# Kernel optimization log

Measured on AMD Instinct MI355X. Metric: run time of the kernel, lower is better.

Reference implementation:

```python
import jax, jax.numpy as jnp
import numpy as np

B, S, H, I, E, TOP_K, NS = 2, 2048, 2048, 1408, 8, 2, 2
SI = I * NS  # shared expert intermediate (intermediate_size * num_shared_expert)
INIT = 0.02


def setup_inputs() -> dict:
    key = jax.random.key(0)
    ks = jax.random.split(key, 9)
    f32 = jnp.float32
    return {
        "hidden_states": jax.random.normal(ks[0], (B, S, H), f32),
        # router classifier: Linear(H, E, bias=False), torch weight [E, H]
        "router_w": (jax.random.normal(ks[1], (E, H), f32) * INIT),
        # grouped experts (SwiGLU, no bias): [E, H, I], [E, H, I], [E, I, H]
        "gate_w": (jax.random.normal(ks[2], (E, H, I), f32) * INIT),
        "up_w": (jax.random.normal(ks[3], (E, H, I), f32) * INIT),
        "down_w": (jax.random.normal(ks[4], (E, I, H), f32) * INIT),
        # shared expert _MLP (bias=True), stored in matmul orientation
        "s_gate_w": (jax.random.normal(ks[5], (H, SI), f32) * INIT),
        "s_gate_b": jnp.zeros((SI,), f32),
        "s_up_w": (jax.random.normal(ks[6], (H, SI), f32) * INIT),
        "s_up_b": jnp.zeros((SI,), f32),
        "s_down_w": (jax.random.normal(ks[7], (SI, H), f32) * INIT),
        "s_down_b": jnp.zeros((H,), f32),
    }


def reference(hidden_states, router_w, gate_w, up_w, down_w,
              s_gate_w, s_gate_b, s_up_w, s_up_b, s_down_w, s_down_b):
    b, s, h = hidden_states.shape
    x = hidden_states.reshape(-1, h)          # [T, H]
    T = x.shape[0]
    num_experts = router_w.shape[0]

    # ---- router: logits -> fp32 softmax -> top-k -> renormalize ----
    logits = x @ router_w.T                   # [T, E]
    probs = jax.nn.softmax(logits.astype(jnp.float32), axis=-1)
    topk_w, topk_idx = jax.lax.top_k(probs, TOP_K)            # [T, K]
    topk_w = topk_w / jnp.sum(topk_w, axis=-1, keepdims=True)
    # dense combine weights [T, E]; zero for unrouted experts
    combine = jnp.zeros((T, num_experts), probs.dtype)
    combine = combine.at[jnp.arange(T)[:, None], topk_idx].add(topk_w)

    # ---- grouped SwiGLU experts; scan over E keeps peak memory at [T, I] ----
    def expert_step(acc, ws):
        gw, uw, dw, ce = ws                  # [H,I], [H,I], [I,H], [T]
        out = (jax.nn.silu(x @ gw) * (x @ uw)) @ dw           # [T, H]
        return acc + ce[:, None].astype(out.dtype) * out, None

    moe_out, _ = jax.lax.scan(expert_step, jnp.zeros_like(x),
                              (gate_w, up_w, down_w, combine.T))

    # ---- shared expert SwiGLU MLP (bias=True), overlapped -> added ----
    shared = (jax.nn.silu(x @ s_gate_w + s_gate_b)
              * (x @ s_up_w + s_up_b)) @ s_down_w + s_down_b

    return (moe_out + shared).reshape(b, s, h)
```

## Files before the change

kernel.cpp:

```cpp
#include <hip/hip_runtime.h>
#include <hip/hip_bf16.h>
#include <stdint.h>

#define T_TOK 4096
#define HDIM  2048
#define IDIM  1408
#define NEXP  8
#define SIDIM 2816
#define GU_CAP 781
#define DN_CAP 568

typedef __bf16 bf16_t;
typedef __bf16 bf16x8 __attribute__((ext_vector_type(8)));
typedef __bf16 bf16x4 __attribute__((ext_vector_type(4)));
typedef float  f32x4  __attribute__((ext_vector_type(4)));

typedef uint32_t __attribute__((address_space(3))) lds_u32;
typedef uint32_t __attribute__((address_space(1))) glb_u32;

__device__ __forceinline__ void glds16(const bf16_t* g, const char* l) {
  __builtin_amdgcn_global_load_lds((const glb_u32*)g, (lds_u32*)l, 16, 0, 0);
}

__device__ __forceinline__ void bar() {
  asm volatile("" ::: "memory");
  __builtin_amdgcn_s_barrier();
  asm volatile("" ::: "memory");
}
#define VMW4 asm volatile("s_waitcnt vmcnt(4)" ::: "memory")
#define VMW0 asm volatile("s_waitcnt vmcnt(0)" ::: "memory")

__device__ __forceinline__ int xcd_swz(int orig, int nwg) {
  int q = nwg >> 3, r = nwg & 7;
  int x = orig & 7, i = orig >> 3;
  return (x < r ? x * (q + 1) : r * (q + 1) + (x - r) * q) + i;
}

__global__ void cvt_x_kernel(const float4* __restrict__ in, bf16x4* __restrict__ out, int n4) {
  int i = blockIdx.x * 256 + threadIdx.x;
  if (i >= n4) return;
  float4 v = in[i];
  bf16x4 o;
  o[0] = (bf16_t)v.x; o[1] = (bf16_t)v.y; o[2] = (bf16_t)v.z; o[3] = (bf16_t)v.w;
  out[i] = o;
}

__global__ void tcvt_kernel(const float* __restrict__ in, bf16_t* __restrict__ out, int R, int C) {
  in  += (size_t)blockIdx.z * R * C;
  out += (size_t)blockIdx.z * R * C;
  __shared__ bf16_t tb[64][72];
  const int r0 = blockIdx.y * 64, c0 = blockIdx.x * 64;
  const int tid = threadIdx.x;
  const int cf4 = tid & 15, rr = tid >> 4;
#pragma unroll
  for (int s = 0; s < 4; ++s) {
    int r = rr + 16 * s;
    float4 v = *(const float4*)(in + (size_t)(r0 + r) * C + c0 + cf4 * 4);
    tb[cf4 * 4 + 0][r] = (bf16_t)v.x;
    tb[cf4 * 4 + 1][r] = (bf16_t)v.y;
    tb[cf4 * 4 + 2][r] = (bf16_t)v.z;
    tb[cf4 * 4 + 3][r] = (bf16_t)v.w;
  }
  __syncthreads();
  const int c = tid >> 2, rb = (tid & 3) * 16;
  bf16x8 w0 = *(const bf16x8*)&tb[c][rb];
  bf16x8 w1 = *(const bf16x8*)&tb[c][rb + 8];
  bf16_t* op = out + (size_t)(c0 + c) * R + r0 + rb;
  *(bf16x8*)op = w0;
  *(bf16x8*)(op + 8) = w1;
}

__global__ void tcvt_gu_kernel(const float* __restrict__ in, bf16_t* __restrict__ out,
                               int R, int C, int which) {
  in  += (size_t)blockIdx.z * R * C;
  out += (size_t)blockIdx.z * (2 * C) * R;
  __shared__ bf16_t tb[64][72];
  const int r0 = blockIdx.y * 64, c0 = blockIdx.x * 64;
  const int tid = threadIdx.x;
  const int cf4 = tid & 15, rr = tid >> 4;
#pragma unroll
  for (int s = 0; s < 4; ++s) {
    int r = rr + 16 * s;
    float4 v = *(const float4*)(in + (size_t)(r0 + r) * C + c0 + cf4 * 4);
    tb[cf4 * 4 + 0][r] = (bf16_t)v.x;
    tb[cf4 * 4 + 1][r] = (bf16_t)v.y;
    tb[cf4 * 4 + 2][r] = (bf16_t)v.z;
    tb[cf4 * 4 + 3][r] = (bf16_t)v.w;
  }
  __syncthreads();
  const int c = tid >> 2, rb = (tid & 3) * 16;
  bf16x8 w0 = *(const bf16x8*)&tb[c][rb];
  bf16x8 w1 = *(const bf16x8*)&tb[c][rb + 8];
  int cg = c0 + c;
  int nprime = ((cg >> 4) << 5) + which * 16 + (cg & 15);
  bf16_t* op = out + (size_t)nprime * R + r0 + rb;
  *(bf16x8*)op = w0;
  *(bf16x8*)(op + 8) = w1;
}

__global__ void router_kernel(const float* __restrict__ x, const float* __restrict__ rw,
                              int* __restrict__ tk_i, float* __restrict__ tk_w,
                              int* __restrict__ counts) {
  int gtid = blockIdx.x * 256 + threadIdx.x;
  int t = gtid >> 6, lane = gtid & 63;
  const float4* xr = (const float4*)(x + (size_t)t * HDIM);
  float acc[NEXP];
#pragma unroll
  for (int e = 0; e < NEXP; e++) acc[e] = 0.f;
  for (int i = lane; i < HDIM / 4; i += 64) {
    float4 xv = xr[i];
#pragma unroll
    for (int e = 0; e < NEXP; e++) {
      float4 wv = ((const float4*)(rw + e * HDIM))[i];
      acc[e] += xv.x * wv.x + xv.y * wv.y + xv.z * wv.z + xv.w * wv.w;
    }
  }
#pragma unroll
  for (int e = 0; e < NEXP; e++)
#pragma unroll
    for (int off = 32; off; off >>= 1) acc[e] += __shfl_down(acc[e], off);
  if (lane == 0) {
    int i1 = 0; float m1 = acc[0];
#pragma unroll
    for (int e = 1; e < NEXP; e++) if (acc[e] > m1) { m1 = acc[e]; i1 = e; }
    int i2 = -1; float m2 = -1e30f;
#pragma unroll
    for (int e = 0; e < NEXP; e++) if (e != i1 && acc[e] > m2) { m2 = acc[e]; i2 = e; }
    float w1 = 1.f / (1.f + __expf(m2 - m1));
    tk_i[t * 2] = i1; tk_i[t * 2 + 1] = i2;
    tk_w[t * 2] = w1; tk_w[t * 2 + 1] = 1.f - w1;
    atomicAdd(&counts[i1], 1); atomicAdd(&counts[i2], 1);
  }
}

__global__ void build_kernel(int* __restrict__ meta) {
  __shared__ int snmt;
  if (threadIdx.x == 0) {
    int o = 0;
    for (int e = 0; e < NEXP; e++) { meta[16 + e] = o; o += meta[e]; }
    meta[24] = o;
    int nmt = 0;
    for (int e = 0; e < NEXP; e++) {
      int nt = (meta[e] + 255) >> 8;
      for (int i = 0; i < nt; i++) { meta[32 + nmt] = e; meta[80 + nmt] = i << 8; nmt++; }
    }
    meta[25] = nmt;
    meta[26] = nmt * 11 + 352;
    meta[27] = nmt * 8 + 256;
    snmt = nmt;
  }
  __syncthreads();
  const int nmt = snmt;
  int4* gt = (int4*)(meta + 128);
  const int ng = nmt * 11 + 352;
  for (int i = threadIdx.x; i < ng; i += 256) {
    int4 v; v.w = 0;
    if (i < nmt * 11) {
      int xt = i / nmt, yt = i - xt * nmt;
      v.x = 0 | (meta[32 + yt] << 1); v.y = meta[80 + yt]; v.z = xt * 256;
    } else {
      int k = i - nmt * 11; int xt = k >> 4, yt = k & 15;
      v.x = 1; v.y = yt * 256; v.z = xt * 256;
    }
    gt[i] = v;
  }
  int4* dt4 = (int4*)(meta + 3328);
  const int nd = nmt * 8 + 256;
  for (int i = threadIdx.x; i < nd; i += 256) {
    int4 v; v.w = 0;
    if (i < nmt * 8) {
      int xt = i / nmt, yt = i - xt * nmt;
      v.x = 0 | (meta[32 + yt] << 1); v.y = meta[80 + yt]; v.z = xt * 256;
    } else {
      int k = i - nmt * 8; int xt = k >> 5, rem = k & 31, ks = rem >> 4, yt = rem & 15;
      v.x = 1 | (ks << 4); v.y = yt * 256; v.z = xt * 256;
    }
    dt4[i] = v;
  }
}

__global__ void scatter_kernel(const int* __restrict__ tk_i, const float* __restrict__ tk_w,
                               int* __restrict__ meta, int* __restrict__ tok_idx,
                               int* __restrict__ tk_slot) {
  int t = blockIdx.x * 256 + threadIdx.x;
  if (t >= T_TOK) return;
#pragma unroll
  for (int k = 0; k < 2; k++) {
    int e = tk_i[t * 2 + k];
    int pos = meta[16 + e] + atomicAdd(&meta[8 + e], 1);
    tok_idx[pos] = t; tk_slot[t * 2 + k] = pos;
  }
}

template <int OP>
__global__ __launch_bounds__(512, 2)
void gemm8p(const bf16_t* __restrict__ A0, const bf16_t* __restrict__ A1,
            const bf16_t* __restrict__ B0, const bf16_t* __restrict__ B1,
            bf16_t* __restrict__ O0, bf16_t* __restrict__ O1, bf16_t* __restrict__ O2,
            const float* __restrict__ bg, const float* __restrict__ bu,
            const int* __restrict__ meta, const int* __restrict__ tok_idx) {
  const int ntiles = meta[OP == 0 ? 26 : 27];
  const int l = blockIdx.x;
  if (l >= ntiles) return;
  const int s = xcd_swz(l, ntiles);
  const int4 tv = ((const int4*)(meta + (OP == 0 ? 128 : 3328)))[s];
  const int kind = tv.x & 1, e = (tv.x >> 1) & 7, ks = (tv.x >> 4) & 1;
  const int row0 = tv.y, n0 = tv.z;

  int cnt, slot0 = 0, strideA, strideB, koffA = 0, koffB = 0;
  const bf16_t *Ab, *Bp;
  constexpr int NKT = (OP == 0) ? (HDIM / 64) : (IDIM / 64);
  if (OP == 0) {
    strideA = HDIM; strideB = HDIM; Ab = A0;
    if (kind == 0) {
      slot0 = meta[16 + e]; cnt = meta[17 + e] - slot0;
      Bp = B0 + (size_t)e * (2 * IDIM) * HDIM;
    } else { cnt = T_TOK; Bp = B1; }
  } else {
    if (kind == 0) {
      slot0 = meta[16 + e]; cnt = meta[17 + e] - slot0;
      Ab = A0; strideA = IDIM;
      Bp = B0 + (size_t)e * HDIM * IDIM; strideB = IDIM;
    } else {
      cnt = T_TOK; Ab = A1; strideA = SIDIM; koffA = ks * IDIM;
      Bp = B1; strideB = SIDIM; koffB = ks * IDIM;
    }
  }

  __shared__ __align__(16) char smem[131072];

  const int t = threadIdx.x;
  const int lane = t & 63, wid = t >> 6;
  const int wr = wid >> 2, wc = wid & 3;
  const int lr = lane & 15, lg = lane >> 4;

  const bf16_t* pA[4]; const bf16_t* pB[4]; int dG[4];
#pragma unroll
  for (int j = 0; j < 4; ++j) {
    int g = j * 512 + t;
    int r = g >> 3;
    int c16 = (g & 7) ^ (r & 7);
    dG[j] = g * 16;
    int rr = row0 + r;
    if (kind == 0 && rr >= cnt) rr = cnt - 1;
    int arow;
    if (OP == 0 && kind == 0) arow = tok_idx[slot0 + rr];
    else if (OP == 1 && kind == 0) arow = slot0 + rr;
    else arow = rr;
    pA[j] = Ab + (size_t)arow * strideA + koffA + c16 * 8;
    pB[j] = Bp + (size_t)(n0 + r) * strideB + koffB + c16 * 8;
  }

  const int cswz0 = ((lg) ^ (lr & 7)) * 16;
  const int cswz1 = ((4 + lg) ^ (lr & 7)) * 16;
  const int aRowB = (wr * 128 + lr) * 128;
  const int bRowB = (wc * 64 + lr) * 128 + 65536;

  f32x4 acc[8][4];
#pragma unroll
  for (int mi = 0; mi < 8; ++mi)
#pragma unroll
    for (int ni = 0; ni < 4; ++ni) acc[mi][ni] = (f32x4)(0.f);

  bf16x8 aL[4][2], aH[4][2], bL[2][2], bH[2][2];

#define ST_A(BUFO, KT, JH) { \
    glds16(pA[(JH)*2]   + (KT)*64, smem + (BUFO) + dG[(JH)*2]); \
    glds16(pA[(JH)*2+1] + (KT)*64, smem + (BUFO) + dG[(JH)*2+1]); }
#define ST_B(BUFO, KT, JH) { \
    glds16(pB[(JH)*2]   + (KT)*64, smem + 65536 + (BUFO) + dG[(JH)*2]); \
    glds16(pB[(JH)*2+1] + (KT)*64, smem + 65536 + (BUFO) + dG[(JH)*2+1]); }
#define RD_A(af, BUFO, MIH) { \
    _Pragma("unroll") for (int mi = 0; mi < 4; ++mi) { \
      af[mi][0] = *(const bf16x8*)(smem + (BUFO) + aRowB + (MIH)*8192 + mi*2048 + cswz0); \
      af[mi][1] = *(const bf16x8*)(smem + (BUFO) + aRowB + (MIH)*8192 + mi*2048 + cswz1); } }
#define RD_B(bf, BUFO, NIH) { \
    _Pragma("unroll") for (int ni = 0; ni < 2; ++ni) { \
      bf[ni][0] = *(const bf16x8*)(smem + (BUFO) + bRowB + (NIH)*4096 + ni*2048 + cswz0); \
      bf[ni][1] = *(const bf16x8*)(smem + (BUFO) + bRowB + (NIH)*4096 + ni*2048 + cswz1); } }
#define MMQ(af, bf, MO, NO) { \
    __builtin_amdgcn_s_setprio(1); \
    _Pragma("unroll") for (int ni = 0; ni < 2; ++ni) \
    _Pragma("unroll") for (int mi = 0; mi < 4; ++mi) { \
      acc[(MO)+mi][(NO)+ni] = __builtin_amdgcn_mfma_f32_16x16x32_bf16(af[mi][0], bf[ni][0], acc[(MO)+mi][(NO)+ni], 0, 0, 0); \
      acc[(MO)+mi][(NO)+ni] = __builtin_amdgcn_mfma_f32_16x16x32_bf16(af[mi][1], bf[ni][1], acc[(MO)+mi][(NO)+ni], 0, 0, 0); } \
    __builtin_amdgcn_s_setprio(0); }
#define KTILE(KT, BO, NBO, W) { \
    RD_A(aL, BO, 0); RD_B(bL, BO, 0); \
    if ((KT) + 1 < NKT) ST_B(NBO, (KT) + 1, 0); \
    bar(); MMQ(aL, bL, 0, 0); bar(); \
    RD_A(aH, BO, 1); \
    if ((KT) + 1 < NKT) ST_B(NBO, (KT) + 1, 1); \
    bar(); MMQ(aH, bL, 4, 0); bar(); \
    RD_B(bH, BO, 1); \
    if ((KT) + 2 < NKT) ST_A(BO, (KT) + 2, 0); \
    bar(); MMQ(aH, bH, 4, 2); bar(); \
    if ((KT) + 2 < NKT) ST_A(BO, (KT) + 2, 1); \
    bar(); MMQ(aL, bH, 0, 2); \
    W; bar(); }

  ST_A(0, 0, 0); ST_A(0, 0, 1);
  ST_B(0, 0, 0); ST_B(0, 0, 1);
  ST_A(32768, 1, 0); ST_A(32768, 1, 1);
  VMW4; bar();

  for (int kt = 0; kt < NKT - 2; kt += 2) {
    KTILE(kt, 0, 32768, VMW4);
    KTILE(kt + 1, 32768, 0, VMW4);
  }
  KTILE(NKT - 2, 0, 32768, VMW0);
  KTILE(NKT - 1, 32768, 0, VMW0);

  if (OP == 0) {
    bf16_t* Ho = kind ? O1 : O0;
    const int HN = kind ? SIDIM : IDIM;
    const int Lbase = n0 >> 1;
#pragma unroll
    for (int mi = 0; mi < 8; ++mi)
#pragma unroll
      for (int j = 0; j < 4; ++j) {
        int row = wr * 128 + mi * 16 + lg * 4 + j;
        int grow = row0 + row;
        if (kind == 0 && grow >= cnt) continue;
        size_t orow = (size_t)((kind ? 0 : slot0) + grow);
#pragma unroll
        for (int nih = 0; nih < 2; ++nih) {
          int Lr = wc * 32 + nih * 16 + lr;
          float g = acc[mi][2 * nih][j];
          float u = acc[mi][2 * nih + 1][j];
          if (kind) { g += bg[Lbase + Lr]; u += bu[Lbase + Lr]; }
          float h = (g / (1.f + __expf(-g))) * u;
          Ho[orow * HN + Lbase + Lr] = (bf16_t)h;
        }
      }
  } else {
    bf16_t* Po = kind ? (ks ? O2 : O1) : O0;
#pragma unroll
    for (int mi = 0; mi < 8; ++mi)
#pragma unroll
      for (int j = 0; j < 4; ++j) {
        int row = wr * 128 + mi * 16 + lg * 4 + j;
        int grow = row0 + row;
        if (kind == 0 && grow >= cnt) continue;
        size_t orow = (size_t)((kind ? 0 : slot0) + grow);
#pragma unroll
        for (int ni = 0; ni < 4; ++ni) {
          int col = n0 + wc * 64 + ni * 16 + lr;
          Po[orow * HDIM + col] = (bf16_t)acc[mi][ni][j];
        }
      }
  }
#undef ST_A
#undef ST_B
#undef RD_A
#undef RD_B
#undef MMQ
#undef KTILE
}

__global__ void combine_kernel(const bf16_t* __restrict__ sh0, const bf16_t* __restrict__ sh1,
                               const bf16_t* __restrict__ rt, const int* __restrict__ tk_slot,
                               const float* __restrict__ tk_w, const float* __restrict__ sdb,
                               float* __restrict__ out) {
  const int t = blockIdx.x;
  const int c = threadIdx.x * 8;
  const int s1 = tk_slot[2 * t], s2 = tk_slot[2 * t + 1];
  const float w1 = tk_w[2 * t], w2 = tk_w[2 * t + 1];
  bf16x8 a = *(const bf16x8*)(sh0 + (size_t)t * HDIM + c);
  bf16x8 b = *(const bf16x8*)(sh1 + (size_t)t * HDIM + c);
  bf16x8 r1 = *(const bf16x8*)(rt + (size_t)s1 * HDIM + c);
  bf16x8 r2 = *(const bf16x8*)(rt + (size_t)s2 * HDIM + c);
  float4 d0 = *(const float4*)(sdb + c);
  float4 d1 = *(const float4*)(sdb + c + 4);
  float o[8];
#pragma unroll
  for (int i = 0; i < 8; i++)
    o[i] = (float)a[i] + (float)b[i] + w1 * (float)r1[i] + w2 * (float)r2[i];
  o[0] += d0.x; o[1] += d0.y; o[2] += d0.z; o[3] += d0.w;
  o[4] += d1.x; o[5] += d1.y; o[6] += d1.z; o[7] += d1.w;
  float4* op = (float4*)(out + (size_t)t * HDIM + c);
  op[0] = make_float4(o[0], o[1], o[2], o[3]);
  op[1] = make_float4(o[4], o[5], o[6], o[7]);
}

extern "C" void kernel_launch(void* const* d_in, const int* in_sizes, int n_in,
                              void* d_out, int out_size, void* d_ws, size_t ws_size,
                              hipStream_t stream) {
  const float* x_f  = (const float*)d_in[0];
  const float* rw   = (const float*)d_in[1];
  const float* gate = (const float*)d_in[2];
  const float* up   = (const float*)d_in[3];
  const float* down = (const float*)d_in[4];
  const float* sgw  = (const float*)d_in[5];
  const float* sgb  = (const float*)d_in[6];
  const float* suw  = (const float*)d_in[7];
  const float* sub  = (const float*)d_in[8];
  const float* sdw  = (const float*)d_in[9];
  const float* sdb  = (const float*)d_in[10];
  float* out = (float*)d_out;

  char* ws = (char*)d_ws;
  size_t off = 0;
  auto alloc = [&](size_t bytes) {
    char* p = ws + off;
    off += (bytes + 255) & ~(size_t)255;
    return p;
  };
  bf16_t* xb    = (bf16_t*)alloc((size_t)T_TOK * HDIM * 2);
  char*   bgur  = alloc((size_t)NEXP * 2 * IDIM * HDIM * 2);
  bf16_t* BguR  = (bf16_t*)bgur;
  bf16_t* BguS  = (bf16_t*)alloc((size_t)2 * SIDIM * HDIM * 2);
  bf16_t* dT    = (bf16_t*)alloc((size_t)NEXP * HDIM * IDIM * 2);
  bf16_t* sdT   = (bf16_t*)alloc((size_t)HDIM * SIDIM * 2);
  bf16_t* hid_r = (bf16_t*)alloc((size_t)(T_TOK * 2) * IDIM * 2);
  bf16_t* hid_s = (bf16_t*)alloc((size_t)T_TOK * SIDIM * 2);
  int*    meta  = (int*)alloc(32768);
  int*    tok_idx = (int*)alloc(8192 * 4);
  int*    tk_slot = (int*)alloc(8192 * 4);
  int*    tk_i    = (int*)alloc((size_t)T_TOK * 2 * 4);
  float*  tk_w2   = (float*)alloc((size_t)T_TOK * 2 * 4);

  bf16_t* rt_p  = (bf16_t*)bgur;
  bf16_t* sh_p0 = (bf16_t*)(bgur + (size_t)8192 * HDIM * 2);
  bf16_t* sh_p1 = (bf16_t*)(bgur + (size_t)8192 * HDIM * 2 + (size_t)T_TOK * HDIM * 2);

  hipMemsetAsync(meta, 0, 64, stream);

  cvt_x_kernel<<<(T_TOK * HDIM / 4) / 256, 256, 0, stream>>>(
      (const float4*)x_f, (bf16x4*)xb, T_TOK * HDIM / 4);

  tcvt_gu_kernel<<<dim3(IDIM / 64, HDIM / 64, NEXP), 256, 0, stream>>>(gate, BguR, HDIM, IDIM, 0);
  tcvt_gu_kernel<<<dim3(IDIM / 64, HDIM / 64, NEXP), 256, 0, stream>>>(up,   BguR, HDIM, IDIM, 1);
  tcvt_gu_kernel<<<dim3(SIDIM / 64, HDIM / 64, 1), 256, 0, stream>>>(sgw, BguS, HDIM, SIDIM, 0);
  tcvt_gu_kernel<<<dim3(SIDIM / 64, HDIM / 64, 1), 256, 0, stream>>>(suw, BguS, HDIM, SIDIM, 1);
  tcvt_kernel<<<dim3(HDIM / 64, IDIM / 64, NEXP), 256, 0, stream>>>(down, dT, IDIM, HDIM);
  tcvt_kernel<<<dim3(HDIM / 64, SIDIM / 64, 1), 256, 0, stream>>>(sdw, sdT, SIDIM, HDIM);

  router_kernel<<<T_TOK / 4, 256, 0, stream>>>(x_f, rw, tk_i, tk_w2, meta);
  build_kernel<<<1, 256, 0, stream>>>(meta);
  scatter_kernel<<<T_TOK / 256, 256, 0, stream>>>(tk_i, tk_w2, meta, tok_idx, tk_slot);

  gemm8p<0><<<GU_CAP, 512, 0, stream>>>(
      xb, nullptr, BguR, BguS, hid_r, hid_s, nullptr, sgb, sub, meta, tok_idx);
  gemm8p<1><<<DN_CAP, 512, 0, stream>>>(
      hid_r, hid_s, dT, sdT, rt_p, sh_p0, sh_p1, nullptr, nullptr, meta, nullptr);
  combine_kernel<<<T_TOK, 256, 0, stream>>>(sh_p0, sh_p1, rt_p, tk_slot, tk_w2, sdb, out);
}
```

Before: 622.0 us.

## Fuse down-weight transposes into gate/up GEMM and x-cast into router

The x fp32→bf16 cast moves into the router kernel, which already reads x, so one pass over x and one launch go away. The two down-projection transpose kernels become extra tile kinds (220 tiles of 64 rows each) in the gate/up GEMM's persistent tile list, so they run alongside the GEMM tiles. The down GEMM now uses a fixed 512-block persistent grid with a grid-stride loop over tiles. This removes several launches and lets the weight transposes overlap GEMM work, at the cost of larger tile metadata, re-encoded tile flags, and transpose tiles that leave MFMA units idle on the CUs that run them.

```diff
diff --git a/kernel.cpp b/kernel.cpp
--- a/kernel.cpp
+++ b/kernel.cpp
@@ -7,8 +7,9 @@
 #define IDIM  1408
 #define NEXP  8
 #define SIDIM 2816
-#define GU_CAP 781
-#define DN_CAP 568
+#define NCVT  220
+#define GU_CAP (781 + NCVT)
+#define DN_GRID 512
 
 typedef __bf16 bf16_t;
 typedef __bf16 bf16x8 __attribute__((ext_vector_type(8)));
@@ -34,40 +35,6 @@
   int q = nwg >> 3, r = nwg & 7;
   int x = orig & 7, i = orig >> 3;
   return (x < r ? x * (q + 1) : r * (q + 1) + (x - r) * q) + i;
-}
-
-__global__ void cvt_x_kernel(const float4* __restrict__ in, bf16x4* __restrict__ out, int n4) {
-  int i = blockIdx.x * 256 + threadIdx.x;
-  if (i >= n4) return;
-  float4 v = in[i];
-  bf16x4 o;
-  o[0] = (bf16_t)v.x; o[1] = (bf16_t)v.y; o[2] = (bf16_t)v.z; o[3] = (bf16_t)v.w;
-  out[i] = o;
-}
-
-__global__ void tcvt_kernel(const float* __restrict__ in, bf16_t* __restrict__ out, int R, int C) {
-  in  += (size_t)blockIdx.z * R * C;
-  out += (size_t)blockIdx.z * R * C;
-  __shared__ bf16_t tb[64][72];
-  const int r0 = blockIdx.y * 64, c0 = blockIdx.x * 64;
-  const int tid = threadIdx.x;
-  const int cf4 = tid & 15, rr = tid >> 4;
-#pragma unroll
-  for (int s = 0; s < 4; ++s) {
-    int r = rr + 16 * s;
-    float4 v = *(const float4*)(in + (size_t)(r0 + r) * C + c0 + cf4 * 4);
-    tb[cf4 * 4 + 0][r] = (bf16_t)v.x;
-    tb[cf4 * 4 + 1][r] = (bf16_t)v.y;
-    tb[cf4 * 4 + 2][r] = (bf16_t)v.z;
-    tb[cf4 * 4 + 3][r] = (bf16_t)v.w;
-  }
-  __syncthreads();
-  const int c = tid >> 2, rb = (tid & 3) * 16;
-  bf16x8 w0 = *(const bf16x8*)&tb[c][rb];
-  bf16x8 w1 = *(const bf16x8*)&tb[c][rb + 8];
-  bf16_t* op = out + (size_t)(c0 + c) * R + r0 + rb;
-  *(bf16x8*)op = w0;
-  *(bf16x8*)(op + 8) = w1;
 }
 
 __global__ void tcvt_gu_kernel(const float* __restrict__ in, bf16_t* __restrict__ out,
@@ -99,16 +66,21 @@
 }
 
 __global__ void router_kernel(const float* __restrict__ x, const float* __restrict__ rw,
+                              bf16_t* __restrict__ xb,
                               int* __restrict__ tk_i, float* __restrict__ tk_w,
                               int* __restrict__ counts) {
   int gtid = blockIdx.x * 256 + threadIdx.x;
   int t = gtid >> 6, lane = gtid & 63;
   const float4* xr = (const float4*)(x + (size_t)t * HDIM);
+  bf16x4* xo = (bf16x4*)(xb + (size_t)t * HDIM);
   float acc[NEXP];
 #pragma unroll
   for (int e = 0; e < NEXP; e++) acc[e] = 0.f;
   for (int i = lane; i < HDIM / 4; i += 64) {
     float4 xv = xr[i];
+    bf16x4 o;
+    o[0] = (bf16_t)xv.x; o[1] = (bf16_t)xv.y; o[2] = (bf16_t)xv.z; o[3] = (bf16_t)xv.w;
+    xo[i] = o;
 #pragma unroll
     for (int e = 0; e < NEXP; e++) {
       float4 wv = ((const float4*)(rw + e * HDIM))[i];
@@ -145,35 +117,40 @@
       for (int i = 0; i < nt; i++) { meta[32 + nmt] = e; meta[80 + nmt] = i << 8; nmt++; }
     }
     meta[25] = nmt;
-    meta[26] = nmt * 11 + 352;
+    meta[26] = nmt * 11 + 352 + NCVT;
     meta[27] = nmt * 8 + 256;
     snmt = nmt;
   }
   __syncthreads();
   const int nmt = snmt;
   int4* gt = (int4*)(meta + 128);
-  const int ng = nmt * 11 + 352;
+  const int ngemm = nmt * 11 + 352;
+  const int ng = ngemm + NCVT;
   for (int i = threadIdx.x; i < ng; i += 256) {
     int4 v; v.w = 0;
     if (i < nmt * 11) {
       int xt = i / nmt, yt = i - xt * nmt;
-      v.x = 0 | (meta[32 + yt] << 1); v.y = meta[80 + yt]; v.z = xt * 256;
-    } else {
+      v.x = 0 | (meta[32 + yt] << 3); v.y = meta[80 + yt]; v.z = xt * 256;
+    } else if (i < ngemm) {
       int k = i - nmt * 11; int xt = k >> 4, yt = k & 15;
       v.x = 1; v.y = yt * 256; v.z = xt * 256;
+    } else {
+      int k = i - ngemm;
+      if (k < 176) { v.x = 2 | ((k / 22) << 3); v.y = (k % 22) * 64; v.z = 0; }
+      else         { v.x = 2 | (1 << 2);        v.y = (k - 176) * 64; v.z = 0; }
     }
     gt[i] = v;
   }
-  int4* dt4 = (int4*)(meta + 3328);
+  int4* dt4 = (int4*)(meta + 4352);
   const int nd = nmt * 8 + 256;
   for (int i = threadIdx.x; i < nd; i += 256) {
     int4 v; v.w = 0;
     if (i < nmt * 8) {
       int xt = i / nmt, yt = i - xt * nmt;
-      v.x = 0 | (meta[32 + yt] << 1); v.y = meta[80 + yt]; v.z = xt * 256;
+      v.x = 0 | (meta[32 + yt] << 3); v.y = meta[80 + yt]; v.z = xt * 256;
     } else {
       int k = i - nmt * 8; int xt = k >> 5, rem = k & 31, ks = rem >> 4, yt = rem & 15;
-      v.x = 1 | (ks << 4); v.y = yt * 256; v.z = xt * 256;
+      v.x = 1 | (ks << 2); v.y = yt * 256; v.z = xt * 256;
     }
     dt4[i] = v;
   }
@@ -198,71 +175,101 @@
             const bf16_t* __restrict__ B0, const bf16_t* __restrict__ B1,
             bf16_t* __restrict__ O0, bf16_t* __restrict__ O1, bf16_t* __restrict__ O2,
             const float* __restrict__ bg, const float* __restrict__ bu,
-            const int* __restrict__ meta, const int* __restrict__ tok_idx) {
+            const int* __restrict__ meta, const int* __restrict__ tok_idx,
+            const float* __restrict__ W0, const float* __restrict__ W1,
+            bf16_t* __restrict__ D0, bf16_t* __restrict__ D1) {
+  __shared__ __align__(16) char smem[131072];
   const int ntiles = meta[OP == 0 ? 26 : 27];
-  const int l = blockIdx.x;
-  if (l >= ntiles) return;
-  const int s = xcd_swz(l, ntiles);
-  const int4 tv = ((const int4*)(meta + (OP == 0 ? 128 : 3328)))[s];
-  const int kind = tv.x & 1, e = (tv.x >> 1) & 7, ks = (tv.x >> 4) & 1;
-  const int row0 = tv.y, n0 = tv.z;
-
-  int cnt, slot0 = 0, strideA, strideB, koffA = 0, koffB = 0;
-  const bf16_t *Ab, *Bp;
-  constexpr int NKT = (OP == 0) ? (HDIM / 64) : (IDIM / 64);
-  if (OP == 0) {
-    strideA = HDIM; strideB = HDIM; Ab = A0;
-    if (kind == 0) {
-      slot0 = meta[16 + e]; cnt = meta[17 + e] - slot0;
-      Bp = B0 + (size_t)e * (2 * IDIM) * HDIM;
-    } else { cnt = T_TOK; Bp = B1; }
-  } else {
-    if (kind == 0) {
-      slot0 = meta[16 + e]; cnt = meta[17 + e] - slot0;
-      Ab = A0; strideA = IDIM;
-      Bp = B0 + (size_t)e * HDIM * IDIM; strideB = IDIM;
-    } else {
-      cnt = T_TOK; Ab = A1; strideA = SIDIM; koffA = ks * IDIM;
-      Bp = B1; strideB = SIDIM; koffB = ks * IDIM;
-    }
-  }
-
-  __shared__ __align__(16) char smem[131072];
-
   const int t = threadIdx.x;
   const int lane = t & 63, wid = t >> 6;
   const int wr = wid >> 2, wc = wid & 3;
   const int lr = lane & 15, lg = lane >> 4;
-
-  const bf16_t* pA[4]; const bf16_t* pB[4]; int dG[4];
-#pragma unroll
-  for (int j = 0; j < 4; ++j) {
-    int g = j * 512 + t;
-    int r = g >> 3;
-    int c16 = (g & 7) ^ (r & 7);
-    dG[j] = g * 16;
-    int rr = row0 + r;
-    if (kind == 0 && rr >= cnt) rr = cnt - 1;
-    int arow;
-    if (OP == 0 && kind == 0) arow = tok_idx[slot0 + rr];
-    else if (OP == 1 && kind == 0) arow = slot0 + rr;
-    else arow = rr;
-    pA[j] = Ab + (size_t)arow * strideA + koffA + c16 * 8;
-    pB[j] = Bp + (size_t)(n0 + r) * strideB + koffB + c16 * 8;
-  }
-
   const int cswz0 = ((lg) ^ (lr & 7)) * 16;
   const int cswz1 = ((4 + lg) ^ (lr & 7)) * 16;
   const int aRowB = (wr * 128 + lr) * 128;
   const int bRowB = (wc * 64 + lr) * 128 + 65536;
-
-  f32x4 acc[8][4];
-#pragma unroll
-  for (int mi = 0; mi < 8; ++mi)
-#pragma unroll
-    for (int ni = 0; ni < 4; ++ni) acc[mi][ni] = (f32x4)(0.f);
-
-  bf16x8 aL[4][2], aH[4][2], bL[2][2], bH[2][2];
+  constexpr int NKT = (OP == 0) ? (HDIM / 64) : (IDIM / 64);
+
+  for (int l = blockIdx.x; l < ntiles; l += gridDim.x) {
+    const int s = xcd_swz(l, ntiles);
+    const int4 tv = ((const int4*)(meta + (OP == 0 ? 128 : 4352)))[s];
+    const int kind = tv.x & 3, e = (tv.x >> 3) & 7, ks = (tv.x >> 2) & 1;
+    const int row0 = tv.y, n0 = tv.z;
+
+    if (OP == 0 && kind == 2) {
+      const float* src; bf16_t* dst; int Rst;
+      if (ks == 0) { src = W0 + ((size_t)e * IDIM + row0) * HDIM;
+                     dst = D0 + (size_t)e * HDIM * IDIM + row0; Rst = IDIM; }
+      else         { src = W1 + (size_t)row0 * HDIM; dst = D1 + row0; Rst = SIDIM; }
+      const int h = t >> 8, tid2 = t & 255;
+      bf16_t (*tb)[72] = (bf16_t(*)[72])(smem + h * 9216);
+      const int cf4 = tid2 & 15, rr2 = tid2 >> 4;
+      const int cc = tid2 >> 2, rb = (tid2 & 3) * 16;
+      for (int it = 0; it < 16; ++it) {
+        const int c0 = it * 128 + h * 64;
+        __syncthreads();
+#pragma unroll
+        for (int sdx = 0; sdx < 4; ++sdx) {
+          int r = rr2 + 16 * sdx;
+          float4 v = *(const float4*)(src + (size_t)r * HDIM + c0 + cf4 * 4);
+          tb[cf4 * 4 + 0][r] = (bf16_t)v.x;
+          tb[cf4 * 4 + 1][r] = (bf16_t)v.y;
+          tb[cf4 * 4 + 2][r] = (bf16_t)v.z;
+          tb[cf4 * 4 + 3][r] = (bf16_t)v.w;
+        }
+        __syncthreads();
+        bf16x8 w0 = *(const bf16x8*)&tb[cc][rb];
+        bf16x8 w1 = *(const bf16x8*)&tb[cc][rb + 8];
+        bf16_t* op = dst + (size_t)(c0 + cc) * Rst + rb;
+        *(bf16x8*)op = w0;
+        *(bf16x8*)(op + 8) = w1;
+      }
+      continue;
+    }
+
+    int cnt, slot0 = 0, strideA, strideB, koffA = 0, koffB = 0;
+    const bf16_t *Ab, *Bp;
+    if (OP == 0) {
+      strideA = HDIM; strideB = HDIM; Ab = A0;
+      if (kind == 0) {
+        slot0 = meta[16 + e]; cnt = meta[17 + e] - slot0;
+        Bp = B0 + (size_t)e * (2 * IDIM) * HDIM;
+      } else { cnt = T_TOK; Bp = B1; }
+    } else {
+      if (kind == 0) {
+        slot0 = meta[16 + e]; cnt = meta[17 + e] - slot0;
+        Ab = A0; strideA = IDIM;
+        Bp = B0 + (size_t)e * HDIM * IDIM; strideB = IDIM;
+      } else {
+        cnt = T_TOK; Ab = A1; strideA = SIDIM; koffA = ks * IDIM;
+        Bp = B1; strideB = SIDIM; koffB = ks * IDIM;
+      }
+    }
+
+    const bf16_t* pA[4]; const bf16_t* pB[4]; int dG[4];
+#pragma unroll
+    for (int j = 0; j < 4; ++j) {
+      int g = j * 512 + t;
+      int r = g >> 3;
+      int c16 = (g & 7) ^ (r & 7);
+      dG[j] = g * 16;
+      int rr = row0 + r;
+      if (kind == 0 && rr >= cnt) rr = cnt - 1;
+      int arow;
+      if (OP == 0 && kind == 0) arow = tok_idx[slot0 + rr];
+      else if (OP == 1 && kind == 0) arow = slot0 + rr;
+      else arow = rr;
+      pA[j] = Ab + (size_t)arow * strideA + koffA + c16 * 8;
+      pB[j] = Bp + (size_t)(n0 + r) * strideB + koffB + c16 * 8;
+    }
+
+    f32x4 acc[8][4];
+#pragma unroll
+    for (int mi = 0; mi < 8; ++mi)
+#pragma unroll
+      for (int ni = 0; ni < 4; ++ni) acc[mi][ni] = (f32x4)(0.f);
+
+    bf16x8 aL[4][2], aH[4][2], bL[2][2], bH[2][2];
 
 #define ST_A(BUFO, KT, JH) { \
     glds16(pA[(JH)*2]   + (KT)*64, smem + (BUFO) + dG[(JH)*2]); \
@@ -299,63 +306,64 @@
     bar(); MMQ(aL, bH, 0, 2); \
     W; bar(); }
 
-  ST_A(0, 0, 0); ST_A(0, 0, 1);
-  ST_B(0, 0, 0); ST_B(0, 0, 1);
-  ST_A(32768, 1, 0); ST_A(32768, 1, 1);
-  VMW4; bar();
-
-  for (int kt = 0; kt < NKT - 2; kt += 2) {
-    KTILE(kt, 0, 32768, VMW4);
-    KTILE(kt + 1, 32768, 0, VMW4);
-  }
-  KTILE(NKT - 2, 0, 32768, VMW0);
-  KTILE(NKT - 1, 32768, 0, VMW0);
-
-  if (OP == 0) {
-    bf16_t* Ho = kind ? O1 : O0;
-    const int HN = kind ? SIDIM : IDIM;
-    const int Lbase = n0 >> 1;
-#pragma unroll
-    for (int mi = 0; mi < 8; ++mi)
-#pragma unroll
-      for (int j = 0; j < 4; ++j) {
-        int row = wr * 128 + mi * 16 + lg * 4 + j;
-        int grow = row0 + row;
-        if (kind == 0 && grow >= cnt) continue;
-        size_t orow = (size_t)((kind ? 0 : slot0) + grow);
-#pragma unroll
-        for (int nih = 0; nih < 2; ++nih) {
-          int Lr = wc * 32 + nih * 16 + lr;
-          float g = acc[mi][2 * nih][j];
-          float u = acc[mi][2 * nih + 1][j];
-          if (kind) { g += bg[Lbase + Lr]; u += bu[Lbase + Lr]; }
-          float h = (g / (1.f + __expf(-g))) * u;
-          Ho[orow * HN + Lbase + Lr] = (bf16_t)h;
+    ST_A(0, 0, 0); ST_A(0, 0, 1);
+    ST_B(0, 0, 0); ST_B(0, 0, 1);
+    ST_A(32768, 1, 0); ST_A(32768, 1, 1);
+    VMW4; bar();
+
+    for (int kt = 0; kt < NKT - 2; kt += 2) {
+      KTILE(kt, 0, 32768, VMW4);
+      KTILE(kt + 1, 32768, 0, VMW4);
+    }
+    KTILE(NKT - 2, 0, 32768, VMW0);
+    KTILE(NKT - 1, 32768, 0, VMW0);
+
+    if (OP == 0) {
+      bf16_t* Ho = kind ? O1 : O0;
+      const int HN = kind ? SIDIM : IDIM;
+      const int Lbase = n0 >> 1;
+#pragma unroll
+      for (int mi = 0; mi < 8; ++mi)
+#pragma unroll
+        for (int j = 0; j < 4; ++j) {
+          int row = wr * 128 + mi * 16 + lg * 4 + j;
+          int grow = row0 + row;
+          if (kind == 0 && grow >= cnt) continue;
+          size_t orow = (size_t)((kind ? 0 : slot0) + grow);
+#pragma unroll
+          for (int nih = 0; nih < 2; ++nih) {
+            int Lr = wc * 32 + nih * 16 + lr;
+            float g = acc[mi][2 * nih][j];
+            float u = acc[mi][2 * nih + 1][j];
+            if (kind) { g += bg[Lbase + Lr]; u += bu[Lbase + Lr]; }
+            float h = (g / (1.f + __expf(-g))) * u;
+            Ho[orow * HN + Lbase + Lr] = (bf16_t)h;
+          }
         }
-      }
-  } else {
-    bf16_t* Po = kind ? (ks ? O2 : O1) : O0;
-#pragma unroll
-    for (int mi = 0; mi < 8; ++mi)
-#pragma unroll
-      for (int j = 0; j < 4; ++j) {
-        int row = wr * 128 + mi * 16 + lg * 4 + j;
-        int grow = row0 + row;
-        if (kind == 0 && grow >= cnt) continue;
-        size_t orow = (size_t)((kind ? 0 : slot0) + grow);
-#pragma unroll
-        for (int ni = 0; ni < 4; ++ni) {
-          int col = n0 + wc * 64 + ni * 16 + lr;
-          Po[orow * HDIM + col] = (bf16_t)acc[mi][ni][j];
+    } else {
+      bf16_t* Po = kind ? (ks ? O2 : O1) : O0;
+#pragma unroll
+      for (int mi = 0; mi < 8; ++mi)
+#pragma unroll
+        for (int j = 0; j < 4; ++j) {
+          int row = wr * 128 + mi * 16 + lg * 4 + j;
+          int grow = row0 + row;
+          if (kind == 0 && grow >= cnt) continue;
+          size_t orow = (size_t)((kind ? 0 : slot0) + grow);
+#pragma unroll
+          for (int ni = 0; ni < 4; ++ni) {
+            int col = n0 + wc * 64 + ni * 16 + lr;
+            Po[orow * HDIM + col] = (bf16_t)acc[mi][ni][j];
+          }
         }
-      }
-  }
+    }
 #undef ST_A
 #undef ST_B
 #undef RD_A
 #undef RD_B
 #undef MMQ
 #undef KTILE
+  }
 }
 
 __global__ void combine_kernel(const bf16_t* __restrict__ sh0, const bf16_t* __restrict__ sh1,
@@ -426,23 +434,20 @@
 
   hipMemsetAsync(meta, 0, 64, stream);
 
-  cvt_x_kernel<<<(T_TOK * HDIM / 4) / 256, 256, 0, stream>>>(
-      (const float4*)x_f, (bf16x4*)xb, T_TOK * HDIM / 4);
-
   tcvt_gu_kernel<<<dim3(IDIM / 64, HDIM / 64, NEXP), 256, 0, stream>>>(gate, BguR, HDIM, IDIM, 0);
   tcvt_gu_kernel<<<dim3(IDIM / 64, HDIM / 64, NEXP), 256, 0, stream>>>(up,   BguR, HDIM, IDIM, 1);
   tcvt_gu_kernel<<<dim3(SIDIM / 64, HDIM / 64, 1), 256, 0, stream>>>(sgw, BguS, HDIM, SIDIM, 0);
   tcvt_gu_kernel<<<dim3(SIDIM / 64, HDIM / 64, 1), 256, 0, stream>>>(suw, BguS, HDIM, SIDIM, 1);
-  tcvt_kernel<<<dim3(HDIM / 64, IDIM / 64, NEXP), 256, 0, stream>>>(down, dT, IDIM, HDIM);
-  tcvt_kernel<<<dim3(HDIM / 64, SIDIM / 64, 1), 256, 0, stream>>>(sdw, sdT, SIDIM, HDIM);
-
-  router_kernel<<<T_TOK / 4, 256, 0, stream>>>(x_f, rw, tk_i, tk_w2, meta);
+
+  router_kernel<<<T_TOK / 4, 256, 0, stream>>>(x_f, rw, xb, tk_i, tk_w2, meta);
   build_kernel<<<1, 256, 0, stream>>>(meta);
   scatter_kernel<<<T_TOK / 256, 256, 0, stream>>>(tk_i, tk_w2, meta, tok_idx, tk_slot);
 
   gemm8p<0><<<GU_CAP, 512, 0, stream>>>(
-      xb, nullptr, BguR, BguS, hid_r, hid_s, nullptr, sgb, sub, meta, tok_idx);
-  gemm8p<1><<<DN_CAP, 512, 0, stream>>>(
-      hid_r, hid_s, dT, sdT, rt_p, sh_p0, sh_p1, nullptr, nullptr, meta, nullptr);
+      xb, nullptr, BguR, BguS, hid_r, hid_s, nullptr, sgb, sub, meta, tok_idx,
+      down, sdw, dT, sdT);
+  gemm8p<1><<<DN_GRID, 512, 0, stream>>>(
+      hid_r, hid_s, dT, sdT, rt_p, sh_p0, sh_p1, nullptr, nullptr, meta, nullptr,
+      nullptr, nullptr, nullptr, nullptr);
   combine_kernel<<<T_TOK, 256, 0, stream>>>(sh_p0, sh_p1, rt_p, tk_slot, tk_w2, sdb, out);
 }
```

New measurement: 760.0 us. 1.22x slower.
